# Performance work log

Measured on AMD Instinct MI355X. Metric: run time of the kernel, lower is better.

Reference implementation:

```python
import jax, jax.numpy as jnp
import numpy as np

ATOM_FDIM = 133
BOND_FDIM = 14
DIM = 512
DEPTH = 4
N_ATOMS = 100000
N_BONDS = 300000
MAX_NB = 6
N_MOLS = 500


def _lin(x, w, b):
    return x @ w + b


def setup_inputs() -> dict:
    key = jax.random.key(0)
    ks = jax.random.split(key, 16)
    s = 0.02
    f_atoms = jax.random.normal(ks[0], (N_ATOMS, ATOM_FDIM), jnp.float32)
    f_bonds = jax.random.normal(ks[1], (N_BONDS, BOND_FDIM), jnp.float32)
    a2a = jax.random.randint(ks[2], (N_ATOMS, MAX_NB), 0, N_ATOMS, jnp.int32)
    a2b = jax.random.randint(ks[3], (N_ATOMS, MAX_NB), 0, N_BONDS, jnp.int32)
    # atom 0 is padding -> assign out-of-range segment id so segment_sum drops it
    ids = np.minimum((np.arange(N_ATOMS) - 1) // ((N_ATOMS - 1) // N_MOLS), N_MOLS - 1)
    ids[0] = N_MOLS
    mol_ids = jnp.asarray(ids, jnp.int32)
    return {
        'f_atoms': f_atoms, 'f_bonds': f_bonds, 'a2a': a2a, 'a2b': a2b,
        'mol_ids': mol_ids, 'n_mols': N_MOLS,
        'W_i_w': jax.random.normal(ks[4], (ATOM_FDIM, DIM), jnp.float32) * s,
        'W_i_b': jnp.zeros((DIM,), jnp.float32),
        'Wh0_w': jax.random.normal(ks[5], (DIM + BOND_FDIM, DIM), jnp.float32) * s,
        'Wh0_b': jnp.zeros((DIM,), jnp.float32),
        'Wh1_w': jax.random.normal(ks[6], (DIM, DIM), jnp.float32) * s,
        'Wh1_b': jnp.zeros((DIM,), jnp.float32),
        'Wh2_w': jax.random.normal(ks[7], (DIM, DIM), jnp.float32) * s,
        'Wh2_b': jnp.zeros((DIM,), jnp.float32),
        'Wah0_w': jax.random.normal(ks[8], (ATOM_FDIM, DIM), jnp.float32) * s,
        'Wah0_b': jnp.zeros((DIM,), jnp.float32),
        'Wah1_w': jax.random.normal(ks[9], (DIM, DIM), jnp.float32) * s,
        'Wah1_b': jnp.zeros((DIM,), jnp.float32),
        'Wah2_w': jax.random.normal(ks[10], (DIM, DIM), jnp.float32) * s,
        'Wah2_b': jnp.zeros((DIM,), jnp.float32),
        'W_o_w': jax.random.normal(ks[11], (2 * DIM, DIM), jnp.float32) * s,
        'W_o_b': jnp.zeros((DIM,), jnp.float32),
    }


def reference(f_atoms, f_bonds, a2a, a2b, mol_ids, n_mols,
              W_i_w, W_i_b, Wh0_w, Wh0_b, Wh1_w, Wh1_b, Wh2_w, Wh2_b,
              Wah0_w, Wah0_b, Wah1_w, Wah1_b, Wah2_w, Wah2_b, W_o_w, W_o_b):
    # input atom hidden; row 0 is padding and is zeroed
    h0 = jax.nn.relu(_lin(f_atoms, W_i_w, W_i_b))        # [A, dim]
    msg = h0.at[0].set(0.0)
    self_msg = msg
    # NOTE: original code shares one modulList across all W_h{i} -> shared weights per depth
    nei_bond_sum = jnp.sum(f_bonds[a2b], axis=1)          # [A, BOND_FDIM] (constant over depths)
    for _ in range(DEPTH):
        nei_atom_sum = jnp.sum(msg[a2a], axis=1)          # [A, dim]
        m = jnp.concatenate([nei_atom_sum, nei_bond_sum], axis=1)  # [A, dim+BOND_FDIM]
        m = _lin(jax.nn.relu(m), Wh0_w, Wh0_b)
        m = _lin(jax.nn.relu(m), Wh1_w, Wh1_b)
        m = _lin(jax.nn.relu(m), Wh2_w, Wh2_b)
        m = self_msg + m
        self_msg = m                                      # kept BEFORE zeroing row 0 (as in torch)
        msg = m.at[0].set(0.0)
    a_message = jnp.sum(msg[a2a], axis=1)                 # [A, dim]
    cc = jax.nn.relu(_lin(f_atoms, Wah0_w, Wah0_b))
    cc = jax.nn.relu(_lin(cc, Wah1_w, Wah1_b))
    cc = jax.nn.relu(_lin(cc, Wah2_w, Wah2_b))
    a_input = jnp.concatenate([cc, a_message], axis=1)    # [A, 2*dim]
    out = jax.nn.relu(_lin(a_input, W_o_w, W_o_b))        # [A, dim]
    # per-molecule sum pooling (a_scope); padding atom has id == n_mols -> dropped
    return jax.ops.segment_sum(out, mol_ids, num_segments=n_mols)
```

## Files before the change

kernel.cpp:

```cpp
#include <hip/hip_runtime.h>
#include <stdint.h>
#include <stddef.h>

typedef __attribute__((ext_vector_type(8))) _Float16 half8;
typedef __attribute__((ext_vector_type(4))) float f32x4;

__device__ __forceinline__ void gload_lds16(const void* g, void* l) {
  __builtin_amdgcn_global_load_lds(
      (const __attribute__((address_space(1))) unsigned int*)g,
      (__attribute__((address_space(3))) unsigned int*)l, 16, 0, 0);
}

enum { EPI_RELU = 0, EPI_INIT = 1, EPI_DEPTH = 2 };

template <int EPI, bool SPLIT, bool ATOMS>
__global__ __launch_bounds__(256) void gemm128(
    const void* __restrict__ A1v, int lda1,
    const _Float16* __restrict__ A2, int lda2, int ksplit,
    const _Float16* __restrict__ Bt,
    const float* __restrict__ bias,
    int M, int K,
    _Float16* __restrict__ out_h, int ldo,
    float* self0,
    _Float16* msg_out)
{
  __shared__ __align__(16) _Float16 Alds[128 * 32];
  __shared__ __align__(16) _Float16 Blds[128 * 32];

  const int t = threadIdx.x;
  const int m0 = blockIdx.x * 128;
  const int n0 = blockIdx.y * 128;

  f32x4 acc[4][4];
#pragma unroll
  for (int i = 0; i < 4; ++i)
#pragma unroll
    for (int j = 0; j < 4; ++j) acc[i][j] = (f32x4){0.f, 0.f, 0.f, 0.f};

  const int lane = t & 63;
  const int w = t >> 6;
  const int wr = (w >> 1) * 64;
  const int wc = (w & 1) * 64;
  const int l16 = lane & 15;
  const int quad = lane >> 4;

  for (int kk = 0; kk < K; kk += 32) {
    __syncthreads();
    if (ATOMS) {
      const float* Af = (const float*)A1v;
#pragma unroll
      for (int h = 0; h < 2; ++h) {
        int i = t + h * 256;
        int r = i >> 2, kg = i & 3;
        int row = m0 + r; if (row > M - 1) row = M - 1;
        int k = kk + kg * 8;
        const float* src = Af + (size_t)row * lda1;
        half8 hv;
#pragma unroll
        for (int e = 0; e < 8; ++e) {
          int kc = k + e;
          hv[e] = (_Float16)(kc < ksplit ? src[kc] : 0.f);
        }
        *(half8*)&Alds[i * 8] = hv;
      }
    } else {
      const _Float16* A1 = (const _Float16*)A1v;
#pragma unroll
      for (int h = 0; h < 2; ++h) {
        int i = t + h * 256;
        int r = i >> 2, kg = i & 3;
        int row = m0 + r; if (row > M - 1) row = M - 1;
        int k = kk + kg * 8;
        const _Float16* src;
        if (SPLIT) {
          src = (k < ksplit) ? (A1 + (size_t)row * lda1 + k)
                             : (A2 + (size_t)row * lda2 + (k - ksplit));
        } else {
          src = A1 + (size_t)row * lda1 + k;
        }
        gload_lds16(src, &Alds[i * 8]);
      }
    }
#pragma unroll
    for (int h = 0; h < 2; ++h) {
      int i = t + h * 256;
      int n = i >> 2, kg = i & 3;
      gload_lds16(Bt + (size_t)(n0 + n) * K + kk + kg * 8, &Blds[i * 8]);
    }
    __syncthreads();

    half8 af[4], bf[4];
#pragma unroll
    for (int mi = 0; mi < 4; ++mi)
      af[mi] = *(const half8*)&Alds[(wr + mi * 16 + l16) * 32 + quad * 8];
#pragma unroll
    for (int ni = 0; ni < 4; ++ni)
      bf[ni] = *(const half8*)&Blds[(wc + ni * 16 + l16) * 32 + quad * 8];
#pragma unroll
    for (int mi = 0; mi < 4; ++mi)
#pragma unroll
      for (int ni = 0; ni < 4; ++ni)
        acc[mi][ni] = __builtin_amdgcn_mfma_f32_16x16x32_f16(af[mi], bf[ni], acc[mi][ni], 0, 0, 0);
  }

#pragma unroll
  for (int mi = 0; mi < 4; ++mi) {
#pragma unroll
    for (int ni = 0; ni < 4; ++ni) {
      int col = n0 + wc + ni * 16 + l16;
      float b = bias[col];
#pragma unroll
      for (int r = 0; r < 4; ++r) {
        int row = m0 + wr + mi * 16 + quad * 4 + r;
        if (row < M) {
          float v = acc[mi][ni][r] + b;
          if (EPI == EPI_RELU) {
            v = fmaxf(v, 0.f);
            out_h[(size_t)row * ldo + col] = (_Float16)v;
          } else if (EPI == EPI_INIT) {
            v = fmaxf(v, 0.f);
            if (row == 0) { msg_out[col] = (_Float16)0.f; self0[col] = 0.f; }
            else msg_out[(size_t)row * 512 + col] = (_Float16)v;
          } else {
            float self = (row == 0) ? self0[col]
                                    : (float)msg_out[(size_t)row * 512 + col];
            v += self;
            if (row == 0) { self0[col] = v; msg_out[col] = (_Float16)0.f; }
            else msg_out[(size_t)row * 512 + col] = (_Float16)v;
          }
        }
      }
    }
  }
}

template <bool SPLIT>
__global__ __launch_bounds__(256) void gemm_wide(
    const _Float16* __restrict__ A1, int lda1,
    const _Float16* __restrict__ A2, int lda2, int ksplit,
    const _Float16* __restrict__ Bt, const float* __restrict__ bias,
    int M, int K,
    _Float16* __restrict__ out_h)
{
  __shared__ __align__(16) _Float16 Alds[64 * 32];
  __shared__ __align__(16) _Float16 Blds[512 * 32];

  const int t = threadIdx.x;
  const int m0 = blockIdx.x * 64;

  f32x4 acc[4][8];
#pragma unroll
  for (int i = 0; i < 4; ++i)
#pragma unroll
    for (int j = 0; j < 8; ++j) acc[i][j] = (f32x4){0.f, 0.f, 0.f, 0.f};

  const int lane = t & 63;
  const int w = t >> 6;
  const int wc = w * 128;
  const int l16 = lane & 15;
  const int quad = lane >> 4;

  for (int kk = 0; kk < K; kk += 32) {
    __syncthreads();
    {
      int r = t >> 2, kg = t & 3;
      int row = m0 + r; if (row > M - 1) row = M - 1;
      int k = kk + kg * 8;
      const _Float16* src;
      if (SPLIT) {
        src = (k < ksplit) ? (A1 + (size_t)row * lda1 + k)
                           : (A2 + (size_t)row * lda2 + (k - ksplit));
      } else {
        src = A1 + (size_t)row * lda1 + k;
      }
      gload_lds16(src, &Alds[t * 8]);
    }
#pragma unroll
    for (int h = 0; h < 8; ++h) {
      int i = t + h * 256;
      int n = i >> 2, kg = i & 3;
      gload_lds16(Bt + (size_t)n * K + kk + kg * 8, &Blds[i * 8]);
    }
    __syncthreads();

    half8 af[4], bf[8];
#pragma unroll
    for (int mi = 0; mi < 4; ++mi)
      af[mi] = *(const half8*)&Alds[(mi * 16 + l16) * 32 + quad * 8];
#pragma unroll
    for (int ni = 0; ni < 8; ++ni)
      bf[ni] = *(const half8*)&Blds[(wc + ni * 16 + l16) * 32 + quad * 8];
#pragma unroll
    for (int mi = 0; mi < 4; ++mi)
#pragma unroll
      for (int ni = 0; ni < 8; ++ni)
        acc[mi][ni] = __builtin_amdgcn_mfma_f32_16x16x32_f16(af[mi], bf[ni], acc[mi][ni], 0, 0, 0);
  }

#pragma unroll
  for (int mi = 0; mi < 4; ++mi) {
#pragma unroll
    for (int ni = 0; ni < 8; ++ni) {
      int col = wc + ni * 16 + l16;
      float b = bias[col];
#pragma unroll
      for (int r = 0; r < 4; ++r) {
        int row = m0 + mi * 16 + quad * 4 + r;
        if (row < M) {
          float v = fmaxf(acc[mi][ni][r] + b, 0.f);
          out_h[(size_t)row * 512 + col] = (_Float16)v;
        }
      }
    }
  }
}

template <bool RELU>
__global__ __launch_bounds__(256) void gather_k(
    const _Float16* __restrict__ msg, const int* __restrict__ a2a,
    _Float16* __restrict__ out, int A)
{
  int t = threadIdx.x;
  int a = blockIdx.x * 4 + (t >> 6);
  if (a >= A) return;
  int g = t & 63;
  const _Float16* base = msg + g * 8;
  float acc[8] = {0, 0, 0, 0, 0, 0, 0, 0};
#pragma unroll
  for (int j = 0; j < 6; ++j) {
    int nb = a2a[a * 6 + j];
    half8 v = *(const half8*)(base + (size_t)nb * 512);
#pragma unroll
    for (int e = 0; e < 8; ++e) acc[e] += (float)v[e];
  }
  half8 o;
#pragma unroll
  for (int e = 0; e < 8; ++e) {
    float x = acc[e];
    if (RELU) x = fmaxf(x, 0.f);
    o[e] = (_Float16)x;
  }
  *(half8*)(out + (size_t)a * 512 + g * 8) = o;
}

__global__ __launch_bounds__(256) void bondsum_k(
    const float* __restrict__ fb, const int* __restrict__ a2b,
    _Float16* __restrict__ bnd, int A)
{
  int idx = blockIdx.x * 256 + threadIdx.x;
  int a = idx >> 5, c = idx & 31;
  if (a >= A) return;
  float s = 0.f;
  if (c < 14) {
#pragma unroll
    for (int j = 0; j < 6; ++j) s += fb[(size_t)a2b[a * 6 + j] * 14 + c];
    s = fmaxf(s, 0.f);
  }
  bnd[(size_t)a * 32 + c] = (_Float16)s;
}

__global__ __launch_bounds__(256) void wcast_k(
    const float* __restrict__ W, _Float16* __restrict__ Wt, int K, int Kpad)
{
  int idx = blockIdx.x * 256 + threadIdx.x;
  if (idx >= 512 * Kpad) return;
  int n = idx / Kpad, k = idx - n * Kpad;
  float v = (k < K) ? W[(size_t)k * 512 + n] : 0.f;
  Wt[idx] = (_Float16)v;
}

__global__ __launch_bounds__(256) void fill_k(float* __restrict__ p, int n, float v) {
  int i = blockIdx.x * 256 + threadIdx.x;
  if (i < n) p[i] = v;
}

__global__ __launch_bounds__(256) void segsum_k(
    const _Float16* __restrict__ x, const int* __restrict__ mol,
    float* __restrict__ out, int A, int n_mols)
{
  int t = threadIdx.x;
  int c = t * 2;
  int a0 = blockIdx.x * 128;
  int aend = a0 + 128; if (aend > A) aend = A;
  float s0 = 0.f, s1 = 0.f;
  int cur = -1;
  for (int a = a0; a < aend; ++a) {
    int m = mol[a];
    if (m != cur) {
      if (cur >= 0 && cur < n_mols) {
        atomicAdd(&out[(size_t)cur * 512 + c], s0);
        atomicAdd(&out[(size_t)cur * 512 + c + 1], s1);
      }
      cur = m; s0 = 0.f; s1 = 0.f;
    }
    const _Float16* row = x + (size_t)a * 512 + c;
    s0 += (float)row[0];
    s1 += (float)row[1];
  }
  if (cur >= 0 && cur < n_mols) {
    atomicAdd(&out[(size_t)cur * 512 + c], s0);
    atomicAdd(&out[(size_t)cur * 512 + c + 1], s1);
  }
}

extern "C" void kernel_launch(void* const* d_in, const int* in_sizes, int n_in,
                              void* d_out, int out_size, void* d_ws, size_t ws_size,
                              hipStream_t stream) {
  const float* f_atoms = (const float*)d_in[0];
  const float* f_bonds = (const float*)d_in[1];
  const int* a2a = (const int*)d_in[2];
  const int* a2b = (const int*)d_in[3];
  const int* mol_ids = (const int*)d_in[4];
  const float* W_i_w  = (const float*)d_in[6];
  const float* W_i_b  = (const float*)d_in[7];
  const float* Wh0_w  = (const float*)d_in[8];
  const float* Wh0_b  = (const float*)d_in[9];
  const float* Wh1_w  = (const float*)d_in[10];
  const float* Wh1_b  = (const float*)d_in[11];
  const float* Wh2_w  = (const float*)d_in[12];
  const float* Wh2_b  = (const float*)d_in[13];
  const float* Wah0_w = (const float*)d_in[14];
  const float* Wah0_b = (const float*)d_in[15];
  const float* Wah1_w = (const float*)d_in[16];
  const float* Wah1_b = (const float*)d_in[17];
  const float* Wah2_w = (const float*)d_in[18];
  const float* Wah2_b = (const float*)d_in[19];
  const float* W_o_w  = (const float*)d_in[20];
  const float* W_o_b  = (const float*)d_in[21];

  const int A = in_sizes[0] / 133;
  const int n_mols = out_size / 512;

  char* ws = (char*)d_ws;
  size_t off = 0;
  auto alloc = [&](size_t bytes) -> void* {
    void* p = ws + off;
    off = (off + bytes + 255) & ~(size_t)255;
    return p;
  };
  const size_t big = (size_t)A * 512 * 2;
  _Float16* MSG = (_Float16*)alloc(big);
  _Float16* Y1  = (_Float16*)alloc(big);
  _Float16* BND = (_Float16*)alloc((size_t)A * 32 * 2);
  _Float16* Wt_i   = (_Float16*)alloc(512 * 160 * 2);
  _Float16* Wt_h0  = (_Float16*)alloc(512 * 544 * 2);
  _Float16* Wt_h1  = (_Float16*)alloc(512 * 512 * 2);
  _Float16* Wt_h2  = (_Float16*)alloc(512 * 512 * 2);
  _Float16* Wt_ah0 = (_Float16*)alloc(512 * 160 * 2);
  _Float16* Wt_ah1 = (_Float16*)alloc(512 * 512 * 2);
  _Float16* Wt_ah2 = (_Float16*)alloc(512 * 512 * 2);
  _Float16* Wt_o   = (_Float16*)alloc(512 * 1024 * 2);
  float* SELF0 = (float*)alloc(512 * 4);
  const size_t req2 = off;
  _Float16* NEI = (_Float16*)alloc(big);
  const size_t req3 = off;

  if (ws_size < req2) {
    fill_k<<<(out_size + 255) / 256, 256, 0, stream>>>(
        (float*)d_out, out_size, (float)(ws_size >> 20));
    return;
  }
  const bool fast3 = ws_size >= req3;

  wcast_k<<<(512 * 160 + 255) / 256, 256, 0, stream>>>(W_i_w, Wt_i, 133, 160);
  wcast_k<<<(512 * 544 + 255) / 256, 256, 0, stream>>>(Wh0_w, Wt_h0, 526, 544);
  wcast_k<<<(512 * 512 + 255) / 256, 256, 0, stream>>>(Wh1_w, Wt_h1, 512, 512);
  wcast_k<<<(512 * 512 + 255) / 256, 256, 0, stream>>>(Wh2_w, Wt_h2, 512, 512);
  wcast_k<<<(512 * 160 + 255) / 256, 256, 0, stream>>>(Wah0_w, Wt_ah0, 133, 160);
  wcast_k<<<(512 * 512 + 255) / 256, 256, 0, stream>>>(Wah1_w, Wt_ah1, 512, 512);
  wcast_k<<<(512 * 512 + 255) / 256, 256, 0, stream>>>(Wah2_w, Wt_ah2, 512, 512);
  wcast_k<<<(512 * 1024 + 255) / 256, 256, 0, stream>>>(W_o_w, Wt_o, 1024, 1024);
  bondsum_k<<<((A * 32) + 255) / 256, 256, 0, stream>>>(f_bonds, a2b, BND, A);

  dim3 g128((A + 127) / 128, 4);
  const int gw = (A + 63) / 64;
  const int gg = (A + 3) / 4;

  gemm128<EPI_INIT, false, true><<<g128, 256, 0, stream>>>(
      f_atoms, 133, nullptr, 0, 133, Wt_i, W_i_b, A, 160, nullptr, 0, SELF0, MSG);

  const _Float16* FINAL;
  if (fast3) {
    for (int d = 0; d < 4; ++d) {
      gather_k<true><<<gg, 256, 0, stream>>>(MSG, a2a, NEI, A);
      gemm128<EPI_RELU, true, false><<<g128, 256, 0, stream>>>(
          NEI, 512, BND, 32, 512, Wt_h0, Wh0_b, A, 544, Y1, 512, nullptr, nullptr);
      gemm128<EPI_RELU, false, false><<<g128, 256, 0, stream>>>(
          Y1, 512, nullptr, 0, 0, Wt_h1, Wh1_b, A, 512, NEI, 512, nullptr, nullptr);
      gemm128<EPI_DEPTH, false, false><<<g128, 256, 0, stream>>>(
          NEI, 512, nullptr, 0, 0, Wt_h2, Wh2_b, A, 512, nullptr, 0, SELF0, MSG);
    }
    gather_k<false><<<gg, 256, 0, stream>>>(MSG, a2a, NEI, A);
    gemm128<EPI_RELU, false, true><<<g128, 256, 0, stream>>>(
        f_atoms, 133, nullptr, 0, 133, Wt_ah0, Wah0_b, A, 160, Y1, 512, nullptr, nullptr);
    gemm128<EPI_RELU, false, false><<<g128, 256, 0, stream>>>(
        Y1, 512, nullptr, 0, 0, Wt_ah1, Wah1_b, A, 512, MSG, 512, nullptr, nullptr);
    gemm128<EPI_RELU, false, false><<<g128, 256, 0, stream>>>(
        MSG, 512, nullptr, 0, 0, Wt_ah2, Wah2_b, A, 512, Y1, 512, nullptr, nullptr);
    gemm128<EPI_RELU, true, false><<<g128, 256, 0, stream>>>(
        Y1, 512, NEI, 512, 512, Wt_o, W_o_b, A, 1024, MSG, 512, nullptr, nullptr);
    FINAL = MSG;
  } else {
    for (int d = 0; d < 4; ++d) {
      gather_k<true><<<gg, 256, 0, stream>>>(MSG, a2a, Y1, A);
      gemm_wide<true><<<gw, 256, 0, stream>>>(
          Y1, 512, BND, 32, 512, Wt_h0, Wh0_b, A, 544, Y1);
      gemm_wide<false><<<gw, 256, 0, stream>>>(
          Y1, 512, nullptr, 0, 0, Wt_h1, Wh1_b, A, 512, Y1);
      gemm128<EPI_DEPTH, false, false><<<g128, 256, 0, stream>>>(
          Y1, 512, nullptr, 0, 0, Wt_h2, Wh2_b, A, 512, nullptr, 0, SELF0, MSG);
    }
    gather_k<false><<<gg, 256, 0, stream>>>(MSG, a2a, Y1, A);
    gemm128<EPI_RELU, false, true><<<g128, 256, 0, stream>>>(
        f_atoms, 133, nullptr, 0, 133, Wt_ah0, Wah0_b, A, 160, MSG, 512, nullptr, nullptr);
    gemm_wide<false><<<gw, 256, 0, stream>>>(
        MSG, 512, nullptr, 0, 0, Wt_ah1, Wah1_b, A, 512, MSG);
    gemm_wide<false><<<gw, 256, 0, stream>>>(
        MSG, 512, nullptr, 0, 0, Wt_ah2, Wah2_b, A, 512, MSG);
    gemm_wide<true><<<gw, 256, 0, stream>>>(
        MSG, 512, Y1, 512, 512, Wt_o, W_o_b, A, 1024, Y1);
    FINAL = Y1;
  }

  fill_k<<<(out_size + 255) / 256, 256, 0, stream>>>((float*)d_out, out_size, 0.f);
  segsum_k<<<(A + 127) / 128, 256, 0, stream>>>(FINAL, mol_ids, (float*)d_out, A, n_mols);
}
```

Before: 4.147 ms.

## Chunk message-passing MLP over row blocks with double-buffered message arrays

Replaces the full-size NEI intermediate with three chunk-sized scratch buffers and processes the per-depth gather plus three GEMMs chunk by chunk. It ping-pongs between two full message buffers so self-message reads come from the old buffer. The point is to keep the intermediates of each chunk in the large last-level cache instead of streaming full 100k×512 activations through HBM between kernels, and to allow the fast GEMM path when workspace is smaller. It adds more kernel launches and smaller grids per chunk, which can cost occupancy and launch overhead.

Result: faster. 3.894 ms (-6.1%).

```diff
diff --git a/kernel.cpp b/kernel.cpp
--- a/kernel.cpp
+++ b/kernel.cpp
@@ -21,8 +21,10 @@
     const float* __restrict__ bias,
     int M, int K,
     _Float16* __restrict__ out_h, int ldo,
+    const _Float16* __restrict__ self_h,
     float* self0,
-    _Float16* msg_out)
+    _Float16* msg_out,
+    int row0)
 {
   __shared__ __align__(16) _Float16 Alds[128 * 32];
   __shared__ __align__(16) _Float16 Blds[128 * 32];
@@ -119,13 +121,13 @@
             out_h[(size_t)row * ldo + col] = (_Float16)v;
           } else if (EPI == EPI_INIT) {
             v = fmaxf(v, 0.f);
-            if (row == 0) { msg_out[col] = (_Float16)0.f; self0[col] = 0.f; }
+            if (row == row0) { msg_out[(size_t)row * 512 + col] = (_Float16)0.f; self0[col] = 0.f; }
             else msg_out[(size_t)row * 512 + col] = (_Float16)v;
           } else {
-            float self = (row == 0) ? self0[col]
-                                    : (float)msg_out[(size_t)row * 512 + col];
+            float self = (row == row0) ? self0[col]
+                                       : (float)self_h[(size_t)row * 512 + col];
             v += self;
-            if (row == 0) { self0[col] = v; msg_out[col] = (_Float16)0.f; }
+            if (row == row0) { self0[col] = v; msg_out[(size_t)row * 512 + col] = (_Float16)0.f; }
             else msg_out[(size_t)row * 512 + col] = (_Float16)v;
           }
         }
@@ -218,17 +220,17 @@
 template <bool RELU>
 __global__ __launch_bounds__(256) void gather_k(
     const _Float16* __restrict__ msg, const int* __restrict__ a2a,
-    _Float16* __restrict__ out, int A)
+    _Float16* __restrict__ out, int rows)
 {
   int t = threadIdx.x;
   int a = blockIdx.x * 4 + (t >> 6);
-  if (a >= A) return;
+  if (a >= rows) return;
   int g = t & 63;
   const _Float16* base = msg + g * 8;
   float acc[8] = {0, 0, 0, 0, 0, 0, 0, 0};
 #pragma unroll
   for (int j = 0; j < 6; ++j) {
-    int nb = a2a[a * 6 + j];
+    int nb = a2a[(size_t)a * 6 + j];
     half8 v = *(const half8*)(base + (size_t)nb * 512);
 #pragma unroll
     for (int e = 0; e < 8; ++e) acc[e] += (float)v[e];
@@ -339,8 +341,8 @@
     return p;
   };
   const size_t big = (size_t)A * 512 * 2;
-  _Float16* MSG = (_Float16*)alloc(big);
-  _Float16* Y1  = (_Float16*)alloc(big);
+  _Float16* MSGA = (_Float16*)alloc(big);
+  _Float16* MSGB = (_Float16*)alloc(big);
   _Float16* BND = (_Float16*)alloc((size_t)A * 32 * 2);
   _Float16* Wt_i   = (_Float16*)alloc(512 * 160 * 2);
   _Float16* Wt_h0  = (_Float16*)alloc(512 * 544 * 2);
@@ -351,16 +353,19 @@
   _Float16* Wt_ah2 = (_Float16*)alloc(512 * 512 * 2);
   _Float16* Wt_o   = (_Float16*)alloc(512 * 1024 * 2);
   float* SELF0 = (float*)alloc(512 * 4);
-  const size_t req2 = off;
-  _Float16* NEI = (_Float16*)alloc(big);
-  const size_t req3 = off;
-
-  if (ws_size < req2) {
+  const size_t fixed = off;
+
+  if (ws_size < fixed) {
     fill_k<<<(out_size + 255) / 256, 256, 0, stream>>>(
         (float*)d_out, out_size, (float)(ws_size >> 20));
     return;
   }
-  const bool fast3 = ws_size >= req3;
+
+  size_t avail = ws_size - fixed;
+  int crows = (int)((avail / 3 - 512) / 1024);
+  crows &= ~127;
+  if (crows > A) crows = (A + 127) & ~127;
+  const bool chunked = crows >= 2048;
 
   wcast_k<<<(512 * 160 + 255) / 256, 256, 0, stream>>>(W_i_w, Wt_i, 133, 160);
   wcast_k<<<(512 * 544 + 255) / 256, 256, 0, stream>>>(Wh0_w, Wt_h0, 526, 544);
@@ -372,56 +377,82 @@
   wcast_k<<<(512 * 1024 + 255) / 256, 256, 0, stream>>>(W_o_w, Wt_o, 1024, 1024);
   bondsum_k<<<((A * 32) + 255) / 256, 256, 0, stream>>>(f_bonds, a2b, BND, A);
 
-  dim3 g128((A + 127) / 128, 4);
-  const int gw = (A + 63) / 64;
-  const int gg = (A + 3) / 4;
-
-  gemm128<EPI_INIT, false, true><<<g128, 256, 0, stream>>>(
-      f_atoms, 133, nullptr, 0, 133, Wt_i, W_i_b, A, 160, nullptr, 0, SELF0, MSG);
-
-  const _Float16* FINAL;
-  if (fast3) {
+  dim3 gfull((A + 127) / 128, 4);
+
+  gemm128<EPI_INIT, false, true><<<gfull, 256, 0, stream>>>(
+      f_atoms, 133, nullptr, 0, 133, Wt_i, W_i_b, A, 160,
+      nullptr, 0, nullptr, SELF0, MSGA, 0);
+
+  if (chunked) {
+    _Float16* NC = (_Float16*)alloc((size_t)crows * 512 * 2);
+    _Float16* YC = (_Float16*)alloc((size_t)crows * 512 * 2);
+    _Float16* ZC = (_Float16*)alloc((size_t)crows * 512 * 2);
+
+    _Float16* MO = MSGA;
+    _Float16* MN = MSGB;
     for (int d = 0; d < 4; ++d) {
-      gather_k<true><<<gg, 256, 0, stream>>>(MSG, a2a, NEI, A);
-      gemm128<EPI_RELU, true, false><<<g128, 256, 0, stream>>>(
-          NEI, 512, BND, 32, 512, Wt_h0, Wh0_b, A, 544, Y1, 512, nullptr, nullptr);
-      gemm128<EPI_RELU, false, false><<<g128, 256, 0, stream>>>(
-          Y1, 512, nullptr, 0, 0, Wt_h1, Wh1_b, A, 512, NEI, 512, nullptr, nullptr);
-      gemm128<EPI_DEPTH, false, false><<<g128, 256, 0, stream>>>(
-          NEI, 512, nullptr, 0, 0, Wt_h2, Wh2_b, A, 512, nullptr, 0, SELF0, MSG);
-    }
-    gather_k<false><<<gg, 256, 0, stream>>>(MSG, a2a, NEI, A);
-    gemm128<EPI_RELU, false, true><<<g128, 256, 0, stream>>>(
-        f_atoms, 133, nullptr, 0, 133, Wt_ah0, Wah0_b, A, 160, Y1, 512, nullptr, nullptr);
-    gemm128<EPI_RELU, false, false><<<g128, 256, 0, stream>>>(
-        Y1, 512, nullptr, 0, 0, Wt_ah1, Wah1_b, A, 512, MSG, 512, nullptr, nullptr);
-    gemm128<EPI_RELU, false, false><<<g128, 256, 0, stream>>>(
-        MSG, 512, nullptr, 0, 0, Wt_ah2, Wah2_b, A, 512, Y1, 512, nullptr, nullptr);
-    gemm128<EPI_RELU, true, false><<<g128, 256, 0, stream>>>(
-        Y1, 512, NEI, 512, 512, Wt_o, W_o_b, A, 1024, MSG, 512, nullptr, nullptr);
-    FINAL = MSG;
+      for (int r0 = 0; r0 < A; r0 += crows) {
+        int rows = A - r0 < crows ? A - r0 : crows;
+        dim3 gg((rows + 127) / 128, 4);
+        int row0 = (r0 == 0) ? 0 : -1;
+        gather_k<true><<<(rows + 3) / 4, 256, 0, stream>>>(MO, a2a + (size_t)r0 * 6, NC, rows);
+        gemm128<EPI_RELU, true, false><<<gg, 256, 0, stream>>>(
+            NC, 512, BND + (size_t)r0 * 32, 32, 512, Wt_h0, Wh0_b, rows, 544,
+            YC, 512, nullptr, nullptr, nullptr, 0);
+        gemm128<EPI_RELU, false, false><<<gg, 256, 0, stream>>>(
+            YC, 512, nullptr, 0, 0, Wt_h1, Wh1_b, rows, 512,
+            ZC, 512, nullptr, nullptr, nullptr, 0);
+        gemm128<EPI_DEPTH, false, false><<<gg, 256, 0, stream>>>(
+            ZC, 512, nullptr, 0, 0, Wt_h2, Wh2_b, rows, 512,
+            nullptr, 0, MO + (size_t)r0 * 512, SELF0, MN + (size_t)r0 * 512, row0);
+      }
+      _Float16* tmp = MO; MO = MN; MN = tmp;
+    }
+    gather_k<false><<<(A + 3) / 4, 256, 0, stream>>>(MO, a2a, MN, A);
+    gemm128<EPI_RELU, false, true><<<gfull, 256, 0, stream>>>(
+        f_atoms, 133, nullptr, 0, 133, Wt_ah0, Wah0_b, A, 160,
+        MO, 512, nullptr, nullptr, nullptr, 0);
+    for (int r0 = 0; r0 < A; r0 += crows) {
+      int rows = A - r0 < crows ? A - r0 : crows;
+      dim3 gg((rows + 127) / 128, 4);
+      gemm128<EPI_RELU, false, false><<<gg, 256, 0, stream>>>(
+          MO + (size_t)r0 * 512, 512, nullptr, 0, 0, Wt_ah1, Wah1_b, rows, 512,
+          YC, 512, nullptr, nullptr, nullptr, 0);
+      gemm128<EPI_RELU, false, false><<<gg, 256, 0, stream>>>(
+          YC, 512, nullptr, 0, 0, Wt_ah2, Wah2_b, rows, 512,
+          ZC, 512, nullptr, nullptr, nullptr, 0);
+      gemm128<EPI_RELU, true, false><<<gg, 256, 0, stream>>>(
+          ZC, 512, MN + (size_t)r0 * 512, 512, 512, Wt_o, W_o_b, rows, 1024,
+          MO + (size_t)r0 * 512, 512, nullptr, nullptr, nullptr, 0);
+    }
+    fill_k<<<(out_size + 255) / 256, 256, 0, stream>>>((float*)d_out, out_size, 0.f);
+    segsum_k<<<(A + 127) / 128, 256, 0, stream>>>(MO, mol_ids, (float*)d_out, A, n_mols);
   } else {
+    _Float16* MSG = MSGA;
+    _Float16* Y1 = MSGB;
+    const int gw = (A + 63) / 64;
+    const int gg = (A + 3) / 4;
     for (int d = 0; d < 4; ++d) {
       gather_k<true><<<gg, 256, 0, stream>>>(MSG, a2a, Y1, A);
       gemm_wide<true><<<gw, 256, 0, stream>>>(
           Y1, 512, BND, 32, 512, Wt_h0, Wh0_b, A, 544, Y1);
       gemm_wide<false><<<gw, 256, 0, stream>>>(
           Y1, 512, nullptr, 0, 0, Wt_h1, Wh1_b, A, 512, Y1);
-      gemm128<EPI_DEPTH, false, false><<<g128, 256, 0, stream>>>(
-          Y1, 512, nullptr, 0, 0, Wt_h2, Wh2_b, A, 512, nullptr, 0, SELF0, MSG);
+      gemm128<EPI_DEPTH, false, false><<<gfull, 256, 0, stream>>>(
+          Y1, 512, nullptr, 0, 0, Wt_h2, Wh2_b, A, 512,
+          nullptr, 0, MSG, SELF0, MSG, 0);
     }
     gather_k<false><<<gg, 256, 0, stream>>>(MSG, a2a, Y1, A);
-    gemm128<EPI_RELU, false, true><<<g128, 256, 0, stream>>>(
-        f_atoms, 133, nullptr, 0, 133, Wt_ah0, Wah0_b, A, 160, MSG, 512, nullptr, nullptr);
+    gemm128<EPI_RELU, false, true><<<gfull, 256, 0, stream>>>(
+        f_atoms, 133, nullptr, 0, 133, Wt_ah0, Wah0_b, A, 160,
+        MSG, 512, nullptr, nullptr, nullptr, 0);
     gemm_wide<false><<<gw, 256, 0, stream>>>(
         MSG, 512, nullptr, 0, 0, Wt_ah1, Wah1_b, A, 512, MSG);
     gemm_wide<false><<<gw, 256, 0, stream>>>(
         MSG, 512, nullptr, 0, 0, Wt_ah2, Wah2_b, A, 512, MSG);
     gemm_wide<true><<<gw, 256, 0, stream>>>(
         MSG, 512, Y1, 512, 512, Wt_o, W_o_b, A, 1024, Y1);
-    FINAL = Y1;
-  }
-
-  fill_k<<<(out_size + 255) / 256, 256, 0, stream>>>((float*)d_out, out_size, 0.f);
-  segsum_k<<<(A + 127) / 128, 256, 0, stream>>>(FINAL, mol_ids, (float*)d_out, A, n_mols);
-}
+    fill_k<<<(out_size + 255) / 256, 256, 0, stream>>>((float*)d_out, out_size, 0.f);
+    segsum_k<<<(A + 127) / 128, 256, 0, stream>>>(Y1, mol_ids, (float*)d_out, A, n_mols);
+  }
+}
```
